# Performance work log

Measured on AMD Instinct MI355X. Metric: run time of the kernel, lower is better.

The kernel has to match this reference:

```python
import jax, jax.numpy as jnp
import numpy as np

N_OPS = 8
TEMP = 1.0
EXP_CLIP = 10.0
EPS = 1e-6
# mask so that the 'none' primitive contributes exactly zero (including its bias term)
BIAS_MASK = jnp.array([0., 1., 1., 1., 1., 1., 1., 1.], dtype=jnp.float32)


def prim_feats(x):
    # x: [B, n_in] -> [B, n_in, K] primitive features
    # protected exp/ln/reciprocal to keep values finite (matches linear_clamp intent in fit())
    return jnp.stack([
        jnp.zeros_like(x),                      # none
        x,                                      # linear
        x * x,                                  # power_two
        x * x * x,                              # power_three
        jnp.exp(jnp.clip(x, -EXP_CLIP, EXP_CLIP)),  # exp
        jnp.log(jnp.abs(x) + EPS),              # ln
        x / (x * x + EPS),                      # reciprocal
        jnp.sin(x),                             # sin
    ], axis=-1)


def darts_layer(x, alphas, scale, bias):
    # alphas/scale/bias: [n_in, n_out, K]; x: [B, n_in]
    w = jax.nn.softmax(alphas / TEMP, axis=-1)          # softmax gating per (i,j)
    feats = prim_feats(x)                               # [B, n_in, K]
    out = jnp.einsum('bik,ijk->bj', feats, w * scale)   # gated sum over inputs and ops
    out = out + jnp.sum(w * bias * BIAS_MASK, axis=(0, 2))
    return out


def setup_inputs() -> dict:
    key = jax.random.key(0)
    ks = jax.random.split(key, 10)
    B, d0, d1, d2, dout, K = 16384, 512, 512, 512, 256, N_OPS
    ir, cs = 0.001, 0.1  # alpha init_range, coefficient scale
    x = jax.random.uniform(ks[0], (B, d0), dtype=jnp.float32) * 2.0 + 0.5
    alphas0 = ir * jax.random.normal(ks[1], (d0, d1, K), dtype=jnp.float32)
    scale0 = cs * jax.random.normal(ks[2], (d0, d1, K), dtype=jnp.float32)
    bias0 = cs * jax.random.normal(ks[3], (d0, d1, K), dtype=jnp.float32)
    alphas1 = ir * jax.random.normal(ks[4], (d1, d2, K), dtype=jnp.float32)
    scale1 = cs * jax.random.normal(ks[5], (d1, d2, K), dtype=jnp.float32)
    bias1 = cs * jax.random.normal(ks[6], (d1, d2, K), dtype=jnp.float32)
    W = jax.random.normal(ks[7], (dout, d2), dtype=jnp.float32) * (1.0 / np.sqrt(d2))
    b = jax.random.normal(ks[8], (dout, 1), dtype=jnp.float32) * 0.01
    return {"x": x, "alphas0": alphas0, "scale0": scale0, "bias0": bias0,
            "alphas1": alphas1, "scale1": scale1, "bias1": bias1, "W": W, "b": b}


def reference(x, alphas0, scale0, bias0, alphas1, scale1, bias1, W, b):
    h = darts_layer(x, alphas0, scale0, bias0)   # [B, 512]
    h = darts_layer(h, alphas1, scale1, bias1)   # [B, 512]
    out = h @ W.T + b.T                          # LinearDARTSLayer: [B, 256]
    return out
```

## Files before the change

kernel.cpp:

```cpp
#include <hip/hip_runtime.h>
#include <string.h>

typedef _Float16 f16x8 __attribute__((ext_vector_type(8)));
typedef float f32x4 __attribute__((ext_vector_type(4)));

#define EXP_CLIP 10.0f
#define FEPS 1e-6f
#define WSCALE 16384.0f
#define WDESCALE (1.0f/16384.0f)
#define PSCALE 1024.0f
#define PDESCALE (1.0f/1024.0f)

__device__ __forceinline__ _Float16 cvh(float v) {
  v = fminf(fmaxf(v, -60000.f), 60000.f);
  return (_Float16)v;
}

__device__ __forceinline__ void gload_lds16(const void* g, void* l) {
  __builtin_amdgcn_global_load_lds(
      (const __attribute__((address_space(1))) void*)g,
      (__attribute__((address_space(3))) void*)l, 16, 0, 0);
}

__device__ __forceinline__ int swz(int row, int colh) {
  return row * 64 + (colh ^ ((row & 7) << 3));
}

__device__ __forceinline__ float prim_eval(int kp, float x) {
  switch (kp) {
    case 0: return x;
    case 1: return x * x;
    case 2: return x * x * x;
    case 3: return __expf(fminf(fmaxf(x, -EXP_CLIP), EXP_CLIP));
    case 4: return __logf(fabsf(x) + FEPS);
    case 5: return x / (x * x + FEPS);
    default: return __sinf(x);
  }
}

__device__ __forceinline__ unsigned char enc_e5m2(float lo) {
  _Float16 lh = (_Float16)lo;
  unsigned short u;
  memcpy(&u, &lh, 2);
  unsigned t = (unsigned)u + 0x7Fu + ((u >> 8) & 1u);
  return (unsigned char)(t >> 8);
}

template <bool EMIT_LO>
__global__ __launch_bounds__(512)
void prep_weights(const float* __restrict__ alphas, const float* __restrict__ scale,
                  const float* __restrict__ bias, _Float16* __restrict__ Wh,
                  _Float16* __restrict__ Wl, float* __restrict__ biasvec) {
  int j = blockIdx.x;
  int i = threadIdx.x;
  size_t base = ((size_t)i * 512 + j) * 8;
  float a[8];
#pragma unroll
  for (int k = 0; k < 8; ++k) a[k] = alphas[base + k];
  float m = a[0];
#pragma unroll
  for (int k = 1; k < 8; ++k) m = fmaxf(m, a[k]);
  float e[8], sum = 0.f;
#pragma unroll
  for (int k = 0; k < 8; ++k) { e[k] = __expf(a[k] - m); sum += e[k]; }
  float inv = 1.f / sum;
  float bp = 0.f;
#pragma unroll
  for (int k = 1; k < 8; ++k) {
    float w = e[k] * inv;
    float ws = fminf(fmaxf(w * scale[base + k] * WSCALE, -60000.f), 60000.f);
    _Float16 wh = (_Float16)ws;
    size_t o = (size_t)j * 3584 + (size_t)(k - 1) * 512 + i;
    Wh[o] = wh;
    if (EMIT_LO) Wl[o] = (_Float16)(ws - (float)wh);
    bp += w * bias[base + k];
  }
  __shared__ float red[512];
  red[i] = bp;
  __syncthreads();
  for (int off = 256; off > 0; off >>= 1) {
    if (i < off) red[i] += red[i + off];
    __syncthreads();
  }
  if (i == 0) biasvec[j] = red[0];
}

__global__ __launch_bounds__(256)
void featurize_hilo(const float* __restrict__ in, _Float16* __restrict__ hi,
                    unsigned char* __restrict__ loB) {
  int t = blockIdx.x * 256 + threadIdx.x;
  int b = t >> 6, g = (t & 63) * 8;
  const float* xp = in + (size_t)b * 512 + g;
  float4 a = *(const float4*)xp;
  float4 c = *(const float4*)(xp + 4);
  float xv[8] = {a.x, a.y, a.z, a.w, c.x, c.y, c.z, c.w};
  _Float16* oh = hi + (size_t)b * 3584 + g;
  unsigned char* ol = loB + (size_t)b * 3584 + g;
#pragma unroll
  for (int kp = 0; kp < 7; ++kp) {
    f16x8 hv;
    unsigned long long lb = 0;
#pragma unroll
    for (int e = 0; e < 8; ++e) {
      float f = prim_eval(kp, xv[e]);
      _Float16 fh = (_Float16)f;
      hv[e] = fh;
      lb |= (unsigned long long)enc_e5m2(f - (float)fh) << (8 * e);
    }
    *(f16x8*)&oh[kp * 512] = hv;
    *(unsigned long long*)&ol[kp * 512] = lb;
  }
}

__global__ __launch_bounds__(256)
void featurize8(const float* __restrict__ in, _Float16* __restrict__ out) {
  int t = blockIdx.x * 256 + threadIdx.x;
  int b = t >> 6, g = (t & 63) * 8;
  const float* xp = in + (size_t)b * 512 + g;
  float4 a = *(const float4*)xp;
  float4 c = *(const float4*)(xp + 4);
  float xv[8] = {a.x, a.y, a.z, a.w, c.x, c.y, c.z, c.w};
  _Float16* o = out + (size_t)b * 3584 + g;
#pragma unroll
  for (int kp = 0; kp < 7; ++kp) {
    f16x8 v;
#pragma unroll
    for (int e = 0; e < 8; ++e) v[e] = cvh(prim_eval(kp, xv[e]));
    *(f16x8*)&o[kp * 512] = v;
  }
}

__global__ __launch_bounds__(256)
void cvt_half_k(const float* __restrict__ in, _Float16* __restrict__ out, int n) {
  int idx = blockIdx.x * 256 + threadIdx.x;
  if (idx < n) out[idx] = (_Float16)(in[idx] * PSCALE);
}

__global__ __launch_bounds__(256)
void gemm_l1_pre(const _Float16* __restrict__ Fhi, const unsigned char* __restrict__ FloB,
                 const _Float16* __restrict__ Wh, const _Float16* __restrict__ Wl,
                 const float* __restrict__ bias, float* __restrict__ H) {
  __shared__ __align__(16) _Float16 AhS[128 * 64];
  __shared__ __align__(16) unsigned char AlB[128 * 64];
  __shared__ __align__(16) _Float16 BhS[128 * 64];
  __shared__ __align__(16) _Float16 BlS[128 * 64];
  const int K = 3584;
  int lin = blockIdx.x;
  int wg = (lin & 7) * 64 + (lin >> 3);
  int bn = wg & 3, bm = wg >> 2;
  int row0 = bm * 128, col0 = bn * 128;
  int tid = threadIdx.x, lane = tid & 63, wave = tid >> 6;
  int wm = wave >> 1, wn = wave & 1;
  int l16 = lane & 15, lh = lane >> 4;
  int sr = lane >> 3, sc = ((lane & 7) * 8) ^ (sr << 3);
  int br = lane >> 2;
  int bp_ = lane & 3;
  int bcs = (bp_ ^ ((br >> 1) & 3)) * 16;

  f32x4 acc[4][4];
#pragma unroll
  for (int m = 0; m < 4; ++m)
#pragma unroll
    for (int n = 0; n < 4; ++n) acc[m][n] = (f32x4){0.f, 0.f, 0.f, 0.f};

  for (int kk0 = 0; kk0 < K; kk0 += 64) {
    const _Float16* Agh = Fhi + (size_t)row0 * K + kk0;
    const unsigned char* Agl = FloB + (size_t)row0 * K + kk0;
    const _Float16* Bgh = Wh + (size_t)col0 * K + kk0;
    const _Float16* Bgl = Wl + (size_t)col0 * K + kk0;
#pragma unroll
    for (int it = 0; it < 4; ++it) {
      int chunk = it * 4 + wave;
      int r = chunk * 8 + sr;
      size_t go = (size_t)r * K + sc;
      gload_lds16(Agh + go, AhS + chunk * 512);
      gload_lds16(Bgh + go, BhS + chunk * 512);
      gload_lds16(Bgl + go, BlS + chunk * 512);
    }
#pragma unroll
    for (int it = 0; it < 2; ++it) {
      int chunk = it * 4 + wave;
      int r = chunk * 16 + br;
      gload_lds16(Agl + (size_t)r * K + bcs, AlB + chunk * 1024);
    }
    __syncthreads();
#pragma unroll
    for (int kc = 0; kc < 2; ++kc) {
      f16x8 ah[4], al[4];
#pragma unroll
      for (int m = 0; m < 4; ++m) {
        int row = wm * 64 + m * 16 + l16;
        ah[m] = *(const f16x8*)&AhS[swz(row, kc * 32 + lh * 8)];
        int cbyte = (kc * 32 + lh * 8) ^ (((row >> 1) & 3) << 4);
        uint2 d = *(const uint2*)&AlB[row * 64 + cbyte];
        union { unsigned u[4]; f16x8 v; } ex;
        ex.u[0] = ((d.x << 8) & 0xFF00u) | ((d.x << 16) & 0xFF000000u);
        ex.u[1] = ((d.x >> 8) & 0xFF00u) | (d.x & 0xFF000000u);
        ex.u[2] = ((d.y << 8) & 0xFF00u) | ((d.y << 16) & 0xFF000000u);
        ex.u[3] = ((d.y >> 8) & 0xFF00u) | (d.y & 0xFF000000u);
        al[m] = ex.v;
      }
#pragma unroll
      for (int n = 0; n < 4; ++n) {
        int ob = swz(wn * 64 + n * 16 + l16, kc * 32 + lh * 8);
        f16x8 bh = *(const f16x8*)&BhS[ob];
        f16x8 bl = *(const f16x8*)&BlS[ob];
#pragma unroll
        for (int m = 0; m < 4; ++m) {
          acc[m][n] = __builtin_amdgcn_mfma_f32_16x16x32_f16(ah[m], bh, acc[m][n], 0, 0, 0);
          acc[m][n] = __builtin_amdgcn_mfma_f32_16x16x32_f16(al[m], bh, acc[m][n], 0, 0, 0);
          acc[m][n] = __builtin_amdgcn_mfma_f32_16x16x32_f16(ah[m], bl, acc[m][n], 0, 0, 0);
        }
      }
    }
    __syncthreads();
  }

#pragma unroll
  for (int m = 0; m < 4; ++m) {
    int row = row0 + wm * 64 + m * 16 + lh * 4;
#pragma unroll
    for (int n = 0; n < 4; ++n) {
      int col = col0 + wn * 64 + n * 16 + l16;
      float bv = bias[col];
#pragma unroll
      for (int r = 0; r < 4; ++r)
        H[(size_t)(row + r) * 512 + col] = acc[m][n][r] * WDESCALE + bv;
    }
  }
}

__global__ __launch_bounds__(256, 2)
void gemm_l1_fused(const float* __restrict__ X, const _Float16* __restrict__ Wh,
                   const _Float16* __restrict__ Wl, const float* __restrict__ bias,
                   float* __restrict__ H) {
  __shared__ __align__(16) _Float16 AhS[128 * 64];
  __shared__ __align__(16) _Float16 AlS[128 * 64];
  __shared__ __align__(16) _Float16 BhS[128 * 64];
  __shared__ __align__(16) _Float16 BlS[128 * 64];
  const int K = 3584;
  int lin = blockIdx.x;
  int wg = (lin & 7) * 64 + (lin >> 3);
  int bn = wg & 3, bm = wg >> 2;
  int row0 = bm * 128, col0 = bn * 128;
  int tid = threadIdx.x, lane = tid & 63, wave = tid >> 6;
  int wm = wave >> 1, wn = wave & 1;
  int l16 = lane & 15, lh = lane >> 4;
  int sr = lane >> 3, sc = ((lane & 7) * 8) ^ (sr << 3);
  int ar = tid >> 3, ac = (tid & 7) * 8;

  f32x4 acc[4][4];
#pragma unroll
  for (int m = 0; m < 4; ++m)
#pragma unroll
    for (int n = 0; n < 4; ++n) acc[m][n] = (f32x4){0.f, 0.f, 0.f, 0.f};

#pragma unroll 1
  for (int kk0 = 0; kk0 < K; kk0 += 64) {
    int kp = kk0 >> 9, i0 = kk0 & 511;
    const _Float16* Bgh = Wh + (size_t)col0 * K + kk0;
    const _Float16* Bgl = Wl + (size_t)col0 * K + kk0;
#pragma unroll
    for (int it = 0; it < 4; ++it) {
      int chunk = it * 4 + wave;
      int r = chunk * 8 + sr;
      gload_lds16(Bgh + (size_t)r * K + sc, BhS + chunk * 512);
      gload_lds16(Bgl + (size_t)r * K + sc, BlS + chunk * 512);
    }
#pragma unroll
    for (int it = 0; it < 4; ++it) {
      int r = it * 32 + ar;
      const float* xp = X + (size_t)(row0 + r) * 512 + i0 + ac;
      float4 x01 = *(const float4*)xp;
      float4 x23 = *(const float4*)(xp + 4);
      float xv[8] = {x01.x, x01.y, x01.z, x01.w, x23.x, x23.y, x23.z, x23.w};
      f16x8 hv, lv;
#pragma unroll
      for (int e = 0; e < 8; ++e) {
        float f = prim_eval(kp, xv[e]);
        _Float16 fh = (_Float16)f;
        hv[e] = fh;
        lv[e] = (_Float16)(f - (float)fh);
      }
      int wo = swz(r, ac);
      *(f16x8*)&AhS[wo] = hv;
      *(f16x8*)&AlS[wo] = lv;
    }
    __syncthreads();
#pragma unroll
    for (int kc = 0; kc < 2; ++kc) {
      f16x8 ah[4], al[4];
#pragma unroll
      for (int m = 0; m < 4; ++m) {
        int off = swz(wm * 64 + m * 16 + l16, kc * 32 + lh * 8);
        ah[m] = *(const f16x8*)&AhS[off];
        al[m] = *(const f16x8*)&AlS[off];
      }
#pragma unroll
      for (int n = 0; n < 4; ++n) {
        int ob = swz(wn * 64 + n * 16 + l16, kc * 32 + lh * 8);
        f16x8 bh = *(const f16x8*)&BhS[ob];
        f16x8 bl = *(const f16x8*)&BlS[ob];
#pragma unroll
        for (int m = 0; m < 4; ++m) {
          acc[m][n] = __builtin_amdgcn_mfma_f32_16x16x32_f16(ah[m], bh, acc[m][n], 0, 0, 0);
          acc[m][n] = __builtin_amdgcn_mfma_f32_16x16x32_f16(al[m], bh, acc[m][n], 0, 0, 0);
          acc[m][n] = __builtin_amdgcn_mfma_f32_16x16x32_f16(ah[m], bl, acc[m][n], 0, 0, 0);
        }
      }
    }
    __syncthreads();
  }

#pragma unroll
  for (int m = 0; m < 4; ++m) {
    int row = row0 + wm * 64 + m * 16 + lh * 4;
#pragma unroll
    for (int n = 0; n < 4; ++n) {
      int col = col0 + wn * 64 + n * 16 + l16;
      float bv = bias[col];
#pragma unroll
      for (int r = 0; r < 4; ++r)
        H[(size_t)(row + r) * 512 + col] = acc[m][n][r] * WDESCALE + bv;
    }
  }
}

template <bool OUT_HALF>
__global__ __launch_bounds__(256)
void gemm_tn(const _Float16* __restrict__ A, const _Float16* __restrict__ BT,
             const float* __restrict__ bias, void* __restrict__ C,
             int M, int N, int K, int nbn_log2, int nwg, float outscale) {
  __shared__ __align__(16) _Float16 Ash[128 * 64];
  __shared__ __align__(16) _Float16 Bsh[128 * 64];
  int lin = blockIdx.x;
  int q = nwg >> 3;
  int wg = (lin & 7) * q + (lin >> 3);
  int bn = wg & ((1 << nbn_log2) - 1);
  int bm = wg >> nbn_log2;
  int row0 = bm * 128, col0 = bn * 128;
  int tid = threadIdx.x, lane = tid & 63, wave = tid >> 6;
  int wm = wave >> 1, wn = wave & 1;
  int l16 = lane & 15, lh = lane >> 4;
  int sr = lane >> 3;
  int sc = ((lane & 7) * 8) ^ (sr << 3);

  f32x4 acc[4][4];
#pragma unroll
  for (int m = 0; m < 4; ++m)
#pragma unroll
    for (int n = 0; n < 4; ++n) acc[m][n] = (f32x4){0.f, 0.f, 0.f, 0.f};

  for (int kk0 = 0; kk0 < K; kk0 += 64) {
    const _Float16* Ag = A + (size_t)row0 * K + kk0;
    const _Float16* Bg = BT + (size_t)col0 * K + kk0;
#pragma unroll
    for (int it = 0; it < 4; ++it) {
      int chunk = it * 4 + wave;
      int r = chunk * 8 + sr;
      gload_lds16(Ag + (size_t)r * K + sc, Ash + chunk * 512);
      gload_lds16(Bg + (size_t)r * K + sc, Bsh + chunk * 512);
    }
    __syncthreads();
#pragma unroll
    for (int kc = 0; kc < 2; ++kc) {
      f16x8 af[4], bf[4];
#pragma unroll
      for (int m = 0; m < 4; ++m)
        af[m] = *(const f16x8*)&Ash[swz(wm * 64 + m * 16 + l16, kc * 32 + lh * 8)];
#pragma unroll
      for (int n = 0; n < 4; ++n)
        bf[n] = *(const f16x8*)&Bsh[swz(wn * 64 + n * 16 + l16, kc * 32 + lh * 8)];
#pragma unroll
      for (int m = 0; m < 4; ++m)
#pragma unroll
        for (int n = 0; n < 4; ++n)
          acc[m][n] = __builtin_amdgcn_mfma_f32_16x16x32_f16(af[m], bf[n], acc[m][n], 0, 0, 0);
    }
    __syncthreads();
  }

#pragma unroll
  for (int m = 0; m < 4; ++m) {
    int row = row0 + wm * 64 + m * 16 + lh * 4;
#pragma unroll
    for (int n = 0; n < 4; ++n) {
      int col = col0 + wn * 64 + n * 16 + l16;
      float bv = bias[col];
#pragma unroll
      for (int r = 0; r < 4; ++r) {
        float v = acc[m][n][r] * outscale + bv;
        if (OUT_HALF)
          ((_Float16*)C)[(size_t)(row + r) * N + col] = cvh(v);
        else
          ((float*)C)[(size_t)(row + r) * N + col] = v;
      }
    }
  }
}

extern "C" void kernel_launch(void* const* d_in, const int* in_sizes, int n_in,
                              void* d_out, int out_size, void* d_ws, size_t ws_size,
                              hipStream_t stream) {
  const float* x  = (const float*)d_in[0];
  const float* a0 = (const float*)d_in[1];
  const float* s0 = (const float*)d_in[2];
  const float* b0 = (const float*)d_in[3];
  const float* a1 = (const float*)d_in[4];
  const float* s1 = (const float*)d_in[5];
  const float* b1 = (const float*)d_in[6];
  const float* W  = (const float*)d_in[7];
  const float* bb = (const float*)d_in[8];

  const int Bn = 16384, D = 512, KK = 3584, DOUT = 256;
  const size_t szF  = (size_t)Bn * KK * 2;
  const size_t szFb = (size_t)Bn * KK;
  const size_t szH  = (size_t)Bn * D * 4;
  const size_t szW  = (size_t)D * KK * 2;
  const size_t szP  = (size_t)DOUT * D * 2;
  const size_t needA = szF + szFb + szH + 3 * szW + szP + 4096;

  if (ws_size >= needA) {
    char* p = (char*)d_ws;
    _Float16*      Fhi  = (_Float16*)p; p += szF;
    unsigned char* FloB = (unsigned char*)p; p += szFb;
    float*    h     = (float*)p;
    _Float16* ghalf = (_Float16*)p; p += szH;
    _Float16* Wh0   = (_Float16*)p; p += szW;
    _Float16* Wl0   = (_Float16*)p; p += szW;
    _Float16* Wh1   = (_Float16*)p; p += szW;
    _Float16* WpT   = (_Float16*)p; p += szP;
    float*    biasv = (float*)p;

    prep_weights<true ><<<dim3(512), dim3(512), 0, stream>>>(a0, s0, b0, Wh0, Wl0, biasv);
    prep_weights<false><<<dim3(512), dim3(512), 0, stream>>>(a1, s1, b1, Wh1, nullptr, biasv + 512);
    cvt_half_k<<<dim3(512), dim3(256), 0, stream>>>(W, WpT, DOUT * D);

    featurize_hilo<<<dim3(Bn * 64 / 256), dim3(256), 0, stream>>>(x, Fhi, FloB);
    gemm_l1_pre<<<dim3(512), dim3(256), 0, stream>>>(Fhi, FloB, Wh0, Wl0, biasv, h);

    featurize8<<<dim3(Bn * 64 / 256), dim3(256), 0, stream>>>(h, Fhi);
    gemm_tn<true><<<dim3(512), dim3(256), 0, stream>>>(Fhi, Wh1, biasv + 512, ghalf,
                                                       Bn, D, KK, 2, 512, WDESCALE);

    gemm_tn<false><<<dim3(256), dim3(256), 0, stream>>>(ghalf, WpT, bb, (float*)d_out,
                                                        Bn, DOUT, D, 1, 256, PDESCALE);
  } else {
    char* p = (char*)d_ws;
    _Float16* Afeat = (_Float16*)p;
    _Float16* Wh0   = (_Float16*)p;
    _Float16* Wl0   = (_Float16*)(p + szW);
    p += szF;
    float*    h     = (float*)p;
    _Float16* ghalf = (_Float16*)p;
    p += szH;
    _Float16* Wh1   = (_Float16*)p; p += szW;
    _Float16* WpT   = (_Float16*)p; p += szP;
    float*    biasv = (float*)p;

    prep_weights<true ><<<dim3(512), dim3(512), 0, stream>>>(a0, s0, b0, Wh0, Wl0, biasv);
    prep_weights<false><<<dim3(512), dim3(512), 0, stream>>>(a1, s1, b1, Wh1, nullptr, biasv + 512);
    cvt_half_k<<<dim3(512), dim3(256), 0, stream>>>(W, WpT, DOUT * D);

    gemm_l1_fused<<<dim3(512), dim3(256), 0, stream>>>(x, Wh0, Wl0, biasv, h);

    featurize8<<<dim3(Bn * 64 / 256), dim3(256), 0, stream>>>(h, Afeat);
    gemm_tn<true><<<dim3(512), dim3(256), 0, stream>>>(Afeat, Wh1, biasv + 512, ghalf,
                                                       Bn, D, KK, 2, 512, WDESCALE);

    gemm_tn<false><<<dim3(256), dim3(256), 0, stream>>>(ghalf, WpT, bb, (float*)d_out,
                                                        Bn, DOUT, D, 1, 256, PDESCALE);
  }
}
```

Measured before the change: 346.7 us.

## Double-buffer LDS tiles and use 8 waves in pre-featurized GEMM kernels

Replaces the single-buffered layer-1 GEMM and the generic TN GEMMs with versions that prefetch the next K-tile into a second LDS buffer while computing on the current one. Each workgroup now has 8 waves instead of 4, each owning a 64x32 output subtile. The change also raises wave priority around the MFMA block and uses a single barrier per iteration. The aim is to hide global-to-LDS load latency behind MFMA work, at the cost of twice the LDS footprint, which may lower occupancy.

```diff
diff --git a/kernel.cpp b/kernel.cpp
--- a/kernel.cpp
+++ b/kernel.cpp
@@ -45,6 +45,13 @@
   unsigned t = (unsigned)u + 0x7Fu + ((u >> 8) & 1u);
   return (unsigned char)(t >> 8);
 }
+
+#define PIPE_TAIL() do { \
+  __builtin_amdgcn_sched_barrier(0); \
+  asm volatile("s_waitcnt vmcnt(0)" ::: "memory"); \
+  __builtin_amdgcn_s_barrier(); \
+  __builtin_amdgcn_sched_barrier(0); \
+} while (0)
 
 template <bool EMIT_LO>
 __global__ __launch_bounds__(512)
@@ -136,63 +143,73 @@
   if (idx < n) out[idx] = (_Float16)(in[idx] * PSCALE);
 }
 
-__global__ __launch_bounds__(256)
-void gemm_l1_pre(const _Float16* __restrict__ Fhi, const unsigned char* __restrict__ FloB,
-                 const _Float16* __restrict__ Wh, const _Float16* __restrict__ Wl,
-                 const float* __restrict__ bias, float* __restrict__ H) {
-  __shared__ __align__(16) _Float16 AhS[128 * 64];
-  __shared__ __align__(16) unsigned char AlB[128 * 64];
-  __shared__ __align__(16) _Float16 BhS[128 * 64];
-  __shared__ __align__(16) _Float16 BlS[128 * 64];
-  const int K = 3584;
+__global__ __launch_bounds__(512, 2)
+void gemm_l1_pipe(const _Float16* __restrict__ Fhi, const unsigned char* __restrict__ FloB,
+                  const _Float16* __restrict__ Wh, const _Float16* __restrict__ Wl,
+                  const float* __restrict__ bias, float* __restrict__ H) {
+  __shared__ __align__(16) _Float16 AhS[2][128 * 64];
+  __shared__ __align__(16) unsigned char AlB[2][128 * 64];
+  __shared__ __align__(16) _Float16 BhS[2][128 * 64];
+  __shared__ __align__(16) _Float16 BlS[2][128 * 64];
+  const int K = 3584, NT = 56;
   int lin = blockIdx.x;
   int wg = (lin & 7) * 64 + (lin >> 3);
   int bn = wg & 3, bm = wg >> 2;
   int row0 = bm * 128, col0 = bn * 128;
   int tid = threadIdx.x, lane = tid & 63, wave = tid >> 6;
-  int wm = wave >> 1, wn = wave & 1;
+  int wm = wave >> 2, wn = wave & 3;
   int l16 = lane & 15, lh = lane >> 4;
   int sr = lane >> 3, sc = ((lane & 7) * 8) ^ (sr << 3);
-  int br = lane >> 2;
-  int bp_ = lane & 3;
+  int br = lane >> 2, bp_ = lane & 3;
   int bcs = (bp_ ^ ((br >> 1) & 3)) * 16;
 
-  f32x4 acc[4][4];
+  const _Float16* Agh = Fhi + (size_t)row0 * K;
+  const unsigned char* Agl = FloB + (size_t)row0 * K;
+  const _Float16* Bgh = Wh + (size_t)col0 * K;
+  const _Float16* Bgl = Wl + (size_t)col0 * K;
+
+  f32x4 acc[4][2];
 #pragma unroll
   for (int m = 0; m < 4; ++m)
 #pragma unroll
-    for (int n = 0; n < 4; ++n) acc[m][n] = (f32x4){0.f, 0.f, 0.f, 0.f};
-
-  for (int kk0 = 0; kk0 < K; kk0 += 64) {
-    const _Float16* Agh = Fhi + (size_t)row0 * K + kk0;
-    const unsigned char* Agl = FloB + (size_t)row0 * K + kk0;
-    const _Float16* Bgh = Wh + (size_t)col0 * K + kk0;
-    const _Float16* Bgl = Wl + (size_t)col0 * K + kk0;
-#pragma unroll
-    for (int it = 0; it < 4; ++it) {
-      int chunk = it * 4 + wave;
+    for (int n = 0; n < 2; ++n) acc[m][n] = (f32x4){0.f, 0.f, 0.f, 0.f};
+
+  auto stage = [&](int t, int p) {
+    int kk = t * 64;
+#pragma unroll
+    for (int it = 0; it < 2; ++it) {
+      int chunk = it * 8 + wave;
       int r = chunk * 8 + sr;
-      size_t go = (size_t)r * K + sc;
-      gload_lds16(Agh + go, AhS + chunk * 512);
-      gload_lds16(Bgh + go, BhS + chunk * 512);
-      gload_lds16(Bgl + go, BlS + chunk * 512);
-    }
-#pragma unroll
-    for (int it = 0; it < 2; ++it) {
-      int chunk = it * 4 + wave;
+      size_t go = (size_t)r * K + kk + sc;
+      gload_lds16(Agh + go, &AhS[p][chunk * 512]);
+      gload_lds16(Bgh + go, &BhS[p][chunk * 512]);
+      gload_lds16(Bgl + go, &BlS[p][chunk * 512]);
+    }
+    {
+      int chunk = wave;
       int r = chunk * 16 + br;
-      gload_lds16(Agl + (size_t)r * K + bcs, AlB + chunk * 1024);
-    }
-    __syncthreads();
+      gload_lds16(Agl + (size_t)r * K + kk + bcs, &AlB[p][chunk * 1024]);
+    }
+  };
+
+  stage(0, 0);
+  PIPE_TAIL();
+
+#pragma unroll 1
+  for (int t = 0; t < NT; ++t) {
+    int p = t & 1;
+    if (t + 1 < NT) stage(t + 1, p ^ 1);
+    __builtin_amdgcn_sched_barrier(0);
+    __builtin_amdgcn_s_setprio(1);
 #pragma unroll
     for (int kc = 0; kc < 2; ++kc) {
       f16x8 ah[4], al[4];
 #pragma unroll
       for (int m = 0; m < 4; ++m) {
         int row = wm * 64 + m * 16 + l16;
-        ah[m] = *(const f16x8*)&AhS[swz(row, kc * 32 + lh * 8)];
+        ah[m] = *(const f16x8*)&AhS[p][swz(row, kc * 32 + lh * 8)];
         int cbyte = (kc * 32 + lh * 8) ^ (((row >> 1) & 3) << 4);
-        uint2 d = *(const uint2*)&AlB[row * 64 + cbyte];
+        uint2 d = *(const uint2*)&AlB[p][row * 64 + cbyte];
         union { unsigned u[4]; f16x8 v; } ex;
         ex.u[0] = ((d.x << 8) & 0xFF00u) | ((d.x << 16) & 0xFF000000u);
         ex.u[1] = ((d.x >> 8) & 0xFF00u) | (d.x & 0xFF000000u);
@@ -201,10 +218,10 @@
         al[m] = ex.v;
       }
 #pragma unroll
-      for (int n = 0; n < 4; ++n) {
-        int ob = swz(wn * 64 + n * 16 + l16, kc * 32 + lh * 8);
-        f16x8 bh = *(const f16x8*)&BhS[ob];
-        f16x8 bl = *(const f16x8*)&BlS[ob];
+      for (int n = 0; n < 2; ++n) {
+        int ob = swz(wn * 32 + n * 16 + l16, kc * 32 + lh * 8);
+        f16x8 bh = *(const f16x8*)&BhS[p][ob];
+        f16x8 bl = *(const f16x8*)&BlS[p][ob];
 #pragma unroll
         for (int m = 0; m < 4; ++m) {
           acc[m][n] = __builtin_amdgcn_mfma_f32_16x16x32_f16(ah[m], bh, acc[m][n], 0, 0, 0);
@@ -213,19 +230,107 @@
         }
       }
     }
-    __syncthreads();
+    __builtin_amdgcn_s_setprio(0);
+    PIPE_TAIL();
   }
 
 #pragma unroll
   for (int m = 0; m < 4; ++m) {
     int row = row0 + wm * 64 + m * 16 + lh * 4;
 #pragma unroll
-    for (int n = 0; n < 4; ++n) {
-      int col = col0 + wn * 64 + n * 16 + l16;
+    for (int n = 0; n < 2; ++n) {
+      int col = col0 + wn * 32 + n * 16 + l16;
       float bv = bias[col];
 #pragma unroll
       for (int r = 0; r < 4; ++r)
         H[(size_t)(row + r) * 512 + col] = acc[m][n][r] * WDESCALE + bv;
+    }
+  }
+}
+
+template <bool OUT_HALF>
+__global__ __launch_bounds__(512, 4)
+void gemm_tn_pipe(const _Float16* __restrict__ A, const _Float16* __restrict__ BT,
+                  const float* __restrict__ bias, void* __restrict__ C,
+                  int M, int N, int K, int nbn_log2, int nwg, float outscale) {
+  __shared__ __align__(16) _Float16 Ash[2][128 * 64];
+  __shared__ __align__(16) _Float16 Bsh[2][128 * 64];
+  int NT = K >> 6;
+  int lin = blockIdx.x;
+  int q = nwg >> 3;
+  int wg = (lin & 7) * q + (lin >> 3);
+  int bn = wg & ((1 << nbn_log2) - 1);
+  int bm = wg >> nbn_log2;
+  int row0 = bm * 128, col0 = bn * 128;
+  int tid = threadIdx.x, lane = tid & 63, wave = tid >> 6;
+  int wm = wave >> 2, wn = wave & 3;
+  int l16 = lane & 15, lh = lane >> 4;
+  int sr = lane >> 3, sc = ((lane & 7) * 8) ^ (sr << 3);
+
+  const _Float16* Ag = A + (size_t)row0 * K;
+  const _Float16* Bg = BT + (size_t)col0 * K;
+
+  f32x4 acc[4][2];
+#pragma unroll
+  for (int m = 0; m < 4; ++m)
+#pragma unroll
+    for (int n = 0; n < 2; ++n) acc[m][n] = (f32x4){0.f, 0.f, 0.f, 0.f};
+
+  auto stage = [&](int t, int p) {
+    int kk = t * 64;
+#pragma unroll
+    for (int it = 0; it < 2; ++it) {
+      int chunk = it * 8 + wave;
+      int r = chunk * 8 + sr;
+      size_t go = (size_t)r * K + kk + sc;
+      gload_lds16(Ag + go, &Ash[p][chunk * 512]);
+      gload_lds16(Bg + go, &Bsh[p][chunk * 512]);
+    }
+  };
+
+  stage(0, 0);
+  PIPE_TAIL();
+
+#pragma unroll 1
+  for (int t = 0; t < NT; ++t) {
+    int p = t & 1;
+    if (t + 1 < NT) stage(t + 1, p ^ 1);
+    __builtin_amdgcn_sched_barrier(0);
+    __builtin_amdgcn_s_setprio(1);
+#pragma unroll
+    for (int kc = 0; kc < 2; ++kc) {
+      f16x8 af[4], bf[2];
+#pragma unroll
+      for (int m = 0; m < 4; ++m)
+        af[m] = *(const f16x8*)&Ash[p][swz(wm * 64 + m * 16 + l16, kc * 32 + lh * 8)];
+#pragma unroll
+      for (int n = 0; n < 2; ++n)
+        bf[n] = *(const f16x8*)&Bsh[p][swz(wn * 32 + n * 16 + l16, kc * 32 + lh * 8)];
+#pragma unroll
+      for (int n = 0; n < 2; ++n)
+#pragma unroll
+        for (int m = 0; m < 4; ++m)
+          acc[m][n] = __builtin_amdgcn_mfma_f32_16x16x32_f16(af[m], bf[n], acc[m][n], 0, 0, 0);
+    }
+    __builtin_amdgcn_s_setprio(0);
+    PIPE_TAIL();
+  }
+
+#pragma unroll
+  for (int m = 0; m < 4; ++m) {
+    int row = row0 + wm * 64 + m * 16 + lh * 4;
+#pragma unroll
+    for (int n = 0; n < 2; ++n) {
+      int col = col0 + wn * 32 + n * 16 + l16;
+      float bv = bias[col];
+#pragma unroll
+      for (int r = 0; r < 4; ++r) {
+        float v = acc[m][n][r] * outscale + bv;
+        if (OUT_HALF)
+          ((_Float16*)C)[(size_t)(row + r) * N + col] = cvh(v);
+        else
+          ((float*)C)[(size_t)(row + r) * N + col] = v;
+      }
     }
   }
 }
@@ -437,14 +542,14 @@
     cvt_half_k<<<dim3(512), dim3(256), 0, stream>>>(W, WpT, DOUT * D);
 
     featurize_hilo<<<dim3(Bn * 64 / 256), dim3(256), 0, stream>>>(x, Fhi, FloB);
-    gemm_l1_pre<<<dim3(512), dim3(256), 0, stream>>>(Fhi, FloB, Wh0, Wl0, biasv, h);
+    gemm_l1_pipe<<<dim3(512), dim3(512), 0, stream>>>(Fhi, FloB, Wh0, Wl0, biasv, h);
 
     featurize8<<<dim3(Bn * 64 / 256), dim3(256), 0, stream>>>(h, Fhi);
-    gemm_tn<true><<<dim3(512), dim3(256), 0, stream>>>(Fhi, Wh1, biasv + 512, ghalf,
-                                                       Bn, D, KK, 2, 512, WDESCALE);
-
-    gemm_tn<false><<<dim3(256), dim3(256), 0, stream>>>(ghalf, WpT, bb, (float*)d_out,
-                                                        Bn, DOUT, D, 1, 256, PDESCALE);
+    gemm_tn_pipe<true><<<dim3(512), dim3(512), 0, stream>>>(Fhi, Wh1, biasv + 512, ghalf,
+                                                            Bn, D, KK, 2, 512, WDESCALE);
+
+    gemm_tn_pipe<false><<<dim3(256), dim3(512), 0, stream>>>(ghalf, WpT, bb, (float*)d_out,
+                                                             Bn, DOUT, D, 1, 256, PDESCALE);
   } else {
     char* p = (char*)d_ws;
     _Float16* Afeat = (_Float16*)p;
```

Result: slower. 397.1 us (+14.5%).
